# Kernel optimization log

Measured on AMD Instinct MI355X. Metric: run time of the kernel, lower is better.

Reference implementation:

```python
import jax, jax.numpy as jnp
import numpy as np

N_NODES = 50000
N_EDGES = 800000
EMBED_ROWS = 100000
NUM_RELS = 16
NUM_BASES = 4
FEAT_DIM = 32
OUT_DIM = 32
ATTN_DIM = 32


def setup_inputs() -> dict:
    key = jax.random.key(0)
    ks = jax.random.split(key, 16)
    inp = {
        'feat': jax.random.normal(ks[0], (N_NODES, FEAT_DIM), jnp.float32),
        'embed_table': jax.random.normal(ks[1], (EMBED_ROWS, FEAT_DIM), jnp.float32),
        'transform': jax.random.normal(ks[2], (FEAT_DIM * 2, OUT_DIM), jnp.float32) * 0.1,
        'weight': jax.random.normal(ks[3], (NUM_BASES, OUT_DIM, OUT_DIM), jnp.float32) * 0.1,
        'w_comp': jax.random.normal(ks[4], (NUM_RELS, NUM_BASES), jnp.float32) * 0.5,
        'self_loop_weight': jax.random.normal(ks[5], (OUT_DIM, OUT_DIM), jnp.float32) * 0.1,
        'A_w': jax.random.normal(ks[6], (2 * OUT_DIM + ATTN_DIM, OUT_DIM), jnp.float32) * 0.1,
        'A_b': jax.random.normal(ks[7], (OUT_DIM,), jnp.float32) * 0.1,
        'B_w': jax.random.normal(ks[8], (OUT_DIM, 1), jnp.float32) * 0.1,
        'B_b': jax.random.normal(ks[9], (1,), jnp.float32) * 0.1,
        'attn_emb': jax.random.normal(ks[10], (NUM_RELS, ATTN_DIM), jnp.float32),
        'idx': jax.random.randint(ks[11], (N_NODES,), 0, EMBED_ROWS, jnp.int32),
        'edge_src': jax.random.randint(ks[12], (N_EDGES,), 0, N_NODES, jnp.int32),
        'edge_dst': jax.random.randint(ks[13], (N_EDGES,), 0, N_NODES, jnp.int32),
        'edge_type': jax.random.randint(ks[14], (N_EDGES,), 0, NUM_RELS, jnp.int32),
    }
    return inp


def reference(feat, embed_table, transform, weight, w_comp, self_loop_weight,
              A_w, A_b, B_w, B_b, attn_emb, idx, edge_src, edge_dst, edge_type):
    n = feat.shape[0]
    # input-layer features: concat(feat, embed[idx]) @ transform -> init_fea [N, D]
    init_fea = jnp.concatenate([feat, embed_table[idx]], axis=1) @ transform
    # basis decomposition: rel_w [R, D, D]
    rel_w = jnp.einsum('rb,bio->rio', w_comp, weight)
    # per-edge gather (is_input_layer & add_transe_emb -> x=src init_fea, y=dst init_fea)
    x = init_fea[edge_src]                      # [E, D]
    y = init_fea[edge_dst]                      # [E, D]
    w_e = rel_w[edge_type]                      # [E, D, D]
    msg = jnp.einsum('ed,edo->eo', x, w_e)      # per-edge bmm (edge weight w = 1)
    # attention MLP: a = sigmoid(B(relu(A([x, y, rel_emb]))))
    e = jnp.concatenate([x, y, attn_emb[edge_type]], axis=1)  # [E, 2D+A]
    a = jax.nn.sigmoid(jax.nn.relu(e @ A_w + A_b) @ B_w + B_b)  # [E, 1]
    # scatter-reduce: h_v = curr_emb_v + sum_{e: dst=v} a_e * msg_e
    agg = jax.ops.segment_sum(a * msg, edge_dst, num_segments=n)
    curr = init_fea @ self_loop_weight
    h = jax.nn.relu(curr + agg)  # activation=relu, bias=None, dropout=0
    # is_input_layer & add_transe_emb: repr = concat(init_fea, h) -> [N, 2, D]
    return jnp.stack([init_fea, h], axis=1)
```

## Files before the change

### kernel.cpp

```cpp
#include <hip/hip_runtime.h>
#include <math.h>

#define NN 50000
#define NE 800000
#define NR 16
#define NEP_MAX (NE + NR * 16)
#define NB 196
#define NBIN 212
#define ABLK 256
#define CHUNK ((NE + ABLK - 1) / ABLK)

typedef __attribute__((ext_vector_type(8))) short short8;
typedef __attribute__((ext_vector_type(4))) float floatx4;

__device__ __forceinline__ unsigned short f2bf(float x) {
    unsigned int u = __float_as_uint(x);
    u += 0x7fffu + ((u >> 16) & 1u);
    return (unsigned short)(u >> 16);
}
__device__ __forceinline__ float bf2f(unsigned short s) {
    return __uint_as_float(((unsigned int)s) << 16);
}

__global__ void k_pre(const float* __restrict__ feat, const float* __restrict__ emb,
                      const float* __restrict__ T, const int* __restrict__ idx,
                      const float* __restrict__ weight, const float* __restrict__ w_comp,
                      const float* __restrict__ A_w, const float* __restrict__ A_b,
                      const float* __restrict__ attn_emb,
                      float* __restrict__ out, unsigned short* __restrict__ init_bf,
                      unsigned short* __restrict__ wfrag, unsigned short* __restrict__ afrag,
                      float* __restrict__ aproj) {
    if (blockIdx.x < 64) {
        int g = blockIdx.x * 256 + threadIdx.x;
        {
            int t = g >> 10, rest = g & 1023;
            int nt = rest >> 9, l = (rest >> 3) & 63, j = rest & 7;
            int k = (l >> 4) * 8 + j, n = (l & 15) + 16 * nt;
            float acc = 0.f;
#pragma unroll
            for (int b = 0; b < 4; b++) acc += w_comp[t * 4 + b] * weight[b * 1024 + k * 32 + n];
            wfrag[g] = f2bf(acc);
        }
        if (g < 2 * 2 * 64 * 8) {
            int ks = g >> 10, rest = g & 1023;
            int nt = rest >> 9, l = (rest >> 3) & 63, j = rest & 7;
            int k = ks * 32 + (l >> 4) * 8 + j, n = (l & 15) + 16 * nt;
            afrag[g] = f2bf(A_w[k * 32 + n]);
        }
        if (g < 16 * 32) {
            int t = g >> 5, j = g & 31;
            float acc = A_b[j];
#pragma unroll
            for (int k = 0; k < 32; k++) acc += attn_emb[t * 32 + k] * A_w[(64 + k) * 32 + j];
            aproj[g] = acc;
        }
        return;
    }
    int i = (blockIdx.x - 64) * 256 + threadIdx.x;
    if (i >= NN) return;
    float v[32], acc[32];
#pragma unroll
    for (int o = 0; o < 32; o++) acc[o] = 0.f;
    const float4* fp = (const float4*)(feat + (size_t)i * 32);
#pragma unroll
    for (int q = 0; q < 8; q++) {
        float4 f = fp[q];
        v[4 * q] = f.x; v[4 * q + 1] = f.y; v[4 * q + 2] = f.z; v[4 * q + 3] = f.w;
    }
#pragma unroll
    for (int d = 0; d < 32; d++) {
        float xd = v[d];
#pragma unroll
        for (int o = 0; o < 32; o++) acc[o] += xd * T[d * 32 + o];
    }
    int row = idx[i];
    const float4* ep = (const float4*)(emb + (size_t)row * 32);
#pragma unroll
    for (int q = 0; q < 8; q++) {
        float4 f = ep[q];
        v[4 * q] = f.x; v[4 * q + 1] = f.y; v[4 * q + 2] = f.z; v[4 * q + 3] = f.w;
    }
#pragma unroll
    for (int d = 0; d < 32; d++) {
        float xd = v[d];
#pragma unroll
        for (int o = 0; o < 32; o++) acc[o] += xd * T[(32 + d) * 32 + o];
    }
    float4* op = (float4*)(out + (size_t)i * 64);
#pragma unroll
    for (int q = 0; q < 8; q++) {
        float4 f;
        f.x = acc[4 * q]; f.y = acc[4 * q + 1]; f.z = acc[4 * q + 2]; f.w = acc[4 * q + 3];
        op[q] = f;
    }
    unsigned int w[16];
#pragma unroll
    for (int q = 0; q < 16; q++)
        w[q] = (unsigned int)f2bf(acc[2 * q]) | ((unsigned int)f2bf(acc[2 * q + 1]) << 16);
    uint4* bp = (uint4*)(init_bf + (size_t)i * 32);
#pragma unroll
    for (int q = 0; q < 4; q++) {
        uint4 u; u.x = w[4 * q]; u.y = w[4 * q + 1]; u.z = w[4 * q + 2]; u.w = w[4 * q + 3];
        bp[q] = u;
    }
}

__global__ void __launch_bounds__(1024) k_count(const int* __restrict__ ed,
                                                const int* __restrict__ et,
                                                int* __restrict__ cpb) {
    __shared__ int lc[NBIN];
    for (int i = threadIdx.x; i < NBIN; i += 1024) lc[i] = 0;
    __syncthreads();
    const int start = blockIdx.x * CHUNK, end = min(start + CHUNK, NE);
    for (int e = start + threadIdx.x; e < end; e += 1024) {
        atomicAdd(&lc[ed[e] >> 8], 1);
        atomicAdd(&lc[NB + et[e]], 1);
    }
    __syncthreads();
    for (int i = threadIdx.x; i < NBIN; i += 1024) cpb[blockIdx.x * NBIN + i] = lc[i];
}

__global__ void __launch_bounds__(256) k_scanB(const int* __restrict__ cpb,
                                               int* __restrict__ cpbx,
                                               int* __restrict__ boff,
                                               int* __restrict__ toff,
                                               int* __restrict__ tend) {
    __shared__ int tot[NBIN];
    int bin = threadIdx.x;
    if (bin < NBIN) {
        int run = 0;
#pragma unroll 8
        for (int c = 0; c < ABLK; c++) {
            int v = cpb[c * NBIN + bin];
            cpbx[c * NBIN + bin] = run;
            run += v;
        }
        tot[bin] = run;
    }
    __syncthreads();
    if (threadIdx.x == 0) {
        int acc = 0;
        for (int b = 0; b < NB; b++) { boff[b] = acc; acc += tot[b]; }
        boff[NB] = acc;
        int t0 = 0;
        for (int t = 0; t < NR; t++) {
            toff[t] = t0;
            tend[t] = t0 + tot[NB + t];
            t0 += ((tot[NB + t] + 15) >> 4) << 4;
        }
        toff[NR] = t0;
    }
}

__global__ void __launch_bounds__(1024) k_scatA(const int* __restrict__ es,
                                                const int* __restrict__ ed,
                                                const int* __restrict__ et,
                                                const int* __restrict__ cpbx,
                                                const int* __restrict__ boff,
                                                const int* __restrict__ toff,
                                                int* __restrict__ tsrc,
                                                int* __restrict__ tdst,
                                                int* __restrict__ bpack) {
    __shared__ int cur[NBIN];
    const int start = blockIdx.x * CHUNK, end = min(start + CHUNK, NE);
    for (int i = threadIdx.x; i < NBIN; i += 1024) {
        int base = (i < NB) ? boff[i] : toff[i - NB];
        cur[i] = base + cpbx[blockIdx.x * NBIN + i];
    }
    __syncthreads();
    for (int e = start + threadIdx.x; e < end; e += 1024) {
        int s = es[e], d = ed[e], t = et[e];
        int q = atomicAdd(&cur[NB + t], 1);
        int slot = atomicAdd(&cur[d >> 8], 1);
        tsrc[q] = s;
        tdst[q] = d;
        bpack[slot] = (q << 8) | (d & 255);
    }
}

__global__ void __launch_bounds__(256) k_fine(const int* __restrict__ boff,
                                              const int* __restrict__ bpack,
                                              int* __restrict__ row_off,
                                              int* __restrict__ p_of_q) {
    __shared__ int h[256], ls[256];
    const int b = blockIdx.x;
    const int s0 = boff[b], s1 = boff[b + 1];
    const int tid = threadIdx.x;
    h[tid] = 0;
    __syncthreads();
    for (int s = s0 + tid; s < s1; s += 256)
        atomicAdd(&h[bpack[s] & 255], 1);
    __syncthreads();
    int v = h[tid];
    ls[tid] = v;
    __syncthreads();
    for (int off = 1; off < 256; off <<= 1) {
        int t = (tid >= off) ? ls[tid - off] : 0;
        __syncthreads();
        ls[tid] += t;
        __syncthreads();
    }
    int excl = ls[tid] - v;
    int node = b * 256 + tid;
    if (node <= NN) row_off[node] = s0 + excl;
    h[tid] = s0 + excl;
    __syncthreads();
    for (int s = s0 + tid; s < s1; s += 256) {
        int pk = bpack[s];
        int p = atomicAdd(&h[pk & 255], 1);
        p_of_q[pk >> 8] = p;
    }
}

__global__ void __launch_bounds__(256) k_msg(
    const unsigned short* __restrict__ wfrag, const unsigned short* __restrict__ afrag,
    const float* __restrict__ aproj, const float* __restrict__ B_w,
    const float* __restrict__ B_b, const int* __restrict__ toff,
    const int* __restrict__ tend, const int* __restrict__ tsrc,
    const int* __restrict__ tdst, const int* __restrict__ p_of_q,
    const unsigned short* __restrict__ init_bf, unsigned short* __restrict__ amsg) {
    const int wave = threadIdx.x >> 6;
    const int lane = threadIdx.x & 63;
    const int q0 = (blockIdx.x * 4 + wave) * 16;
    if (q0 >= toff[NR]) return;
    int t = 0;
#pragma unroll
    for (int i = 1; i < NR; i++) t += (q0 >= toff[i]) ? 1 : 0;
    t = __builtin_amdgcn_readfirstlane(t);
    const int te = tend[t];
    const int m = lane & 15, quad = lane >> 4;
    const int qa = q0 + m;
    const bool va = qa < te;
    int src = va ? tsrc[qa] : 0;
    int dst = va ? tdst[qa] : 0;
    short8 xa = *(const short8*)(init_bf + (size_t)src * 32 + quad * 8);
    short8 ya = *(const short8*)(init_bf + (size_t)dst * 32 + quad * 8);
    short8 wb0 = *(const short8*)(wfrag + (size_t)((t * 2 + 0) * 64 + lane) * 8);
    short8 wb1 = *(const short8*)(wfrag + (size_t)((t * 2 + 1) * 64 + lane) * 8);
    short8 a00 = *(const short8*)(afrag + (size_t)((0 * 2 + 0) * 64 + lane) * 8);
    short8 a01 = *(const short8*)(afrag + (size_t)((0 * 2 + 1) * 64 + lane) * 8);
    short8 a10 = *(const short8*)(afrag + (size_t)((1 * 2 + 0) * 64 + lane) * 8);
    short8 a11 = *(const short8*)(afrag + (size_t)((1 * 2 + 1) * 64 + lane) * 8);
    floatx4 z4 = {0.f, 0.f, 0.f, 0.f};
    floatx4 mc0 = __builtin_amdgcn_mfma_f32_16x16x32_bf16(xa, wb0, z4, 0, 0, 0);
    floatx4 mc1 = __builtin_amdgcn_mfma_f32_16x16x32_bf16(xa, wb1, z4, 0, 0, 0);
    floatx4 hc0 = __builtin_amdgcn_mfma_f32_16x16x32_bf16(xa, a00, z4, 0, 0, 0);
    hc0 = __builtin_amdgcn_mfma_f32_16x16x32_bf16(ya, a10, hc0, 0, 0, 0);
    floatx4 hc1 = __builtin_amdgcn_mfma_f32_16x16x32_bf16(xa, a01, z4, 0, 0, 0);
    hc1 = __builtin_amdgcn_mfma_f32_16x16x32_bf16(ya, a11, hc1, 0, 0, 0);
    const int col = m;
    float ap0 = aproj[t * 32 + col], ap1 = aproj[t * 32 + 16 + col];
    float bw0 = B_w[col], bw1 = B_w[col + 16];
    float bb = B_b[0];
    float part[4];
#pragma unroll
    for (int r = 0; r < 4; r++)
        part[r] = fmaxf(hc0[r] + ap0, 0.f) * bw0 + fmaxf(hc1[r] + ap1, 0.f) * bw1;
#pragma unroll
    for (int s = 1; s < 16; s <<= 1) {
#pragma unroll
        for (int r = 0; r < 4; r++) part[r] += __shfl_xor(part[r], s, 64);
    }
#pragma unroll
    for (int r = 0; r < 4; r++) {
        int qe = q0 + quad * 4 + r;
        if (qe < te) {
            int pe = p_of_q[qe];
            float a = 1.f / (1.f + __expf(-(part[r] + bb)));
            amsg[(size_t)pe * 32 + col] = f2bf(a * mc0[r]);
            amsg[(size_t)pe * 32 + col + 16] = f2bf(a * mc1[r]);
        }
    }
}

__global__ void __launch_bounds__(256) k_agg(
    const int* __restrict__ row_off, const unsigned short* __restrict__ amsg,
    const float* __restrict__ S, float* __restrict__ out) {
    int tid = threadIdx.x;
    int v = blockIdx.x * 64 + (tid >> 2);
    if (v >= NN) return;
    int c0 = (tid & 3) * 8;
    float acc[8];
#pragma unroll
    for (int j = 0; j < 8; j++) acc[j] = 0.f;
    int p0 = row_off[v], p1 = row_off[v + 1];
    for (int p = p0; p < p1; p++) {
        short8 mv = *(const short8*)(amsg + (size_t)p * 32 + c0);
#pragma unroll
        for (int j = 0; j < 8; j++) acc[j] += bf2f((unsigned short)mv[j]);
    }
    float x[32];
    const float4* xp = (const float4*)(out + (size_t)v * 64);
#pragma unroll
    for (int q = 0; q < 8; q++) {
        float4 f = xp[q];
        x[4 * q] = f.x; x[4 * q + 1] = f.y; x[4 * q + 2] = f.z; x[4 * q + 3] = f.w;
    }
#pragma unroll
    for (int d = 0; d < 32; d++) {
        float xd = x[d];
#pragma unroll
        for (int j = 0; j < 8; j++) acc[j] += xd * S[d * 32 + c0 + j];
    }
    float4* op = (float4*)(out + (size_t)v * 64 + 32 + c0);
#pragma unroll
    for (int q = 0; q < 2; q++) {
        float4 f;
        f.x = fmaxf(acc[4 * q], 0.f);
        f.y = fmaxf(acc[4 * q + 1], 0.f);
        f.z = fmaxf(acc[4 * q + 2], 0.f);
        f.w = fmaxf(acc[4 * q + 3], 0.f);
        op[q] = f;
    }
}

extern "C" void kernel_launch(void* const* d_in, const int* in_sizes, int n_in,
                              void* d_out, int out_size, void* d_ws, size_t ws_size,
                              hipStream_t stream) {
    const float* feat      = (const float*)d_in[0];
    const float* embed     = (const float*)d_in[1];
    const float* transform = (const float*)d_in[2];
    const float* weight    = (const float*)d_in[3];
    const float* w_comp    = (const float*)d_in[4];
    const float* self_w    = (const float*)d_in[5];
    const float* A_w       = (const float*)d_in[6];
    const float* A_b       = (const float*)d_in[7];
    const float* B_w       = (const float*)d_in[8];
    const float* B_b       = (const float*)d_in[9];
    const float* attn_emb  = (const float*)d_in[10];
    const int*   idx       = (const int*)d_in[11];
    const int*   edge_src  = (const int*)d_in[12];
    const int*   edge_dst  = (const int*)d_in[13];
    const int*   edge_type = (const int*)d_in[14];
    float* out = (float*)d_out;

    char* ws = (char*)d_ws;
    unsigned short* amsg    = (unsigned short*)ws;
    int*            bpack   = (int*)ws;
    unsigned short* init_bf = (unsigned short*)(ws + (size_t)NEP_MAX * 64);
    unsigned short* wfrag   = (unsigned short*)((char*)init_bf + 3200000);
    unsigned short* afrag   = (unsigned short*)((char*)wfrag + 32768);
    float*          aproj   = (float*)((char*)afrag + 4096);
    int* ip       = (int*)((char*)aproj + 2048);
    int* toff     = ip;              ip += 32;
    int* tend     = ip;              ip += 16;
    int* boff     = ip;              ip += 200;
    int* cpb      = ip;              ip += ABLK * NBIN;
    int* cpbx     = ip;              ip += ABLK * NBIN;
    int* row_off  = ip;              ip += NN + 1;
    int* tsrc     = ip;              ip += NEP_MAX;
    int* tdst     = ip;              ip += NEP_MAX;
    int* p_of_q   = ip;              ip += NEP_MAX;

    k_pre<<<260, 256, 0, stream>>>(feat, embed, transform, idx, weight, w_comp,
                                   A_w, A_b, attn_emb, out, init_bf, wfrag, afrag, aproj);
    k_count<<<ABLK, 1024, 0, stream>>>(edge_dst, edge_type, cpb);
    k_scanB<<<1, 256, 0, stream>>>(cpb, cpbx, boff, toff, tend);
    k_scatA<<<ABLK, 1024, 0, stream>>>(edge_src, edge_dst, edge_type, cpbx, boff, toff,
                                       tsrc, tdst, bpack);
    k_fine<<<NB, 256, 0, stream>>>(boff, bpack, row_off, p_of_q);
    const int tiles = NEP_MAX / 16;
    k_msg<<<(tiles + 3) / 4, 256, 0, stream>>>(wfrag, afrag, aproj, B_w, B_b,
                                               toff, tend, tsrc, tdst, p_of_q,
                                               init_bf, amsg);
    k_agg<<<(NN + 63) / 64, 256, 0, stream>>>(row_off, amsg, self_w, out);
}
```

Baseline: 214.4 us.

## Fuse message and aggregation per 64-node bucket with shared-memory atomics

Replaces the type-sorted edge layout, the fine per-node sort, the bf16 message buffer and the separate aggregation kernel with one kernel per 64-destination bucket. It computes the messages for all four bases with MFMA, combines them with per-edge w_comp, and accumulates into shared memory with atomics. It also folds the dst-bin counting into the preprocessing launch and packs src, local dst and type into one int. This removes several kernels and large intermediate global traffic, at the cost of four times the basis MFMAs and shared-memory atomic contention. The packed form assumes src fits in 16 bits, but node ids go up to 50000, which is below 65536, so it holds.

```diff
diff --git a/kernel.cpp b/kernel.cpp
--- a/kernel.cpp
+++ b/kernel.cpp
@@ -4,9 +4,8 @@
 #define NN 50000
 #define NE 800000
 #define NR 16
-#define NEP_MAX (NE + NR * 16)
-#define NB 196
-#define NBIN 212
+#define BNODE 64
+#define NBC 782
 #define ABLK 256
 #define CHUNK ((NE + ABLK - 1) / ABLK)
 
@@ -18,28 +17,35 @@
     u += 0x7fffu + ((u >> 16) & 1u);
     return (unsigned short)(u >> 16);
 }
-__device__ __forceinline__ float bf2f(unsigned short s) {
-    return __uint_as_float(((unsigned int)s) << 16);
-}
-
-__global__ void k_pre(const float* __restrict__ feat, const float* __restrict__ emb,
-                      const float* __restrict__ T, const int* __restrict__ idx,
-                      const float* __restrict__ weight, const float* __restrict__ w_comp,
-                      const float* __restrict__ A_w, const float* __restrict__ A_b,
-                      const float* __restrict__ attn_emb,
-                      float* __restrict__ out, unsigned short* __restrict__ init_bf,
-                      unsigned short* __restrict__ wfrag, unsigned short* __restrict__ afrag,
-                      float* __restrict__ aproj) {
+
+__global__ void __launch_bounds__(256) k_pre(
+    const float* __restrict__ feat, const float* __restrict__ emb,
+    const float* __restrict__ T, const int* __restrict__ idx,
+    const float* __restrict__ weight, const float* __restrict__ A_w,
+    const float* __restrict__ A_b, const float* __restrict__ attn_emb,
+    const int* __restrict__ ed,
+    float* __restrict__ out, unsigned short* __restrict__ init_bf,
+    unsigned short* __restrict__ bfrag, unsigned short* __restrict__ afrag,
+    float* __restrict__ aproj, int* __restrict__ cpb) {
+    if (blockIdx.x >= 260) {
+        __shared__ int lc[NBC];
+        const int cb = blockIdx.x - 260;
+        for (int i = threadIdx.x; i < NBC; i += 256) lc[i] = 0;
+        __syncthreads();
+        const int start = cb * CHUNK, end = min(start + CHUNK, NE);
+        for (int e = start + threadIdx.x; e < end; e += 256)
+            atomicAdd(&lc[ed[e] >> 6], 1);
+        __syncthreads();
+        for (int i = threadIdx.x; i < NBC; i += 256) cpb[cb * NBC + i] = lc[i];
+        return;
+    }
     if (blockIdx.x < 64) {
         int g = blockIdx.x * 256 + threadIdx.x;
-        {
-            int t = g >> 10, rest = g & 1023;
-            int nt = rest >> 9, l = (rest >> 3) & 63, j = rest & 7;
-            int k = (l >> 4) * 8 + j, n = (l & 15) + 16 * nt;
-            float acc = 0.f;
-#pragma unroll
-            for (int b = 0; b < 4; b++) acc += w_comp[t * 4 + b] * weight[b * 1024 + k * 32 + n];
-            wfrag[g] = f2bf(acc);
+        if (g < 4 * 2 * 64 * 8) {
+            int b2 = g >> 10, rest = g & 1023;
+            int h = rest >> 9, l = (rest >> 3) & 63, j = rest & 7;
+            int k = (l >> 4) * 8 + j, n = (l & 15) + 16 * h;
+            bfrag[g] = f2bf(weight[b2 * 1024 + k * 32 + n]);
         }
         if (g < 2 * 2 * 64 * 8) {
             int ks = g >> 10, rest = g & 1023;
@@ -105,34 +111,16 @@
     }
 }
 
-__global__ void __launch_bounds__(1024) k_count(const int* __restrict__ ed,
-                                                const int* __restrict__ et,
-                                                int* __restrict__ cpb) {
-    __shared__ int lc[NBIN];
-    for (int i = threadIdx.x; i < NBIN; i += 1024) lc[i] = 0;
-    __syncthreads();
-    const int start = blockIdx.x * CHUNK, end = min(start + CHUNK, NE);
-    for (int e = start + threadIdx.x; e < end; e += 1024) {
-        atomicAdd(&lc[ed[e] >> 8], 1);
-        atomicAdd(&lc[NB + et[e]], 1);
-    }
-    __syncthreads();
-    for (int i = threadIdx.x; i < NBIN; i += 1024) cpb[blockIdx.x * NBIN + i] = lc[i];
-}
-
 __global__ void __launch_bounds__(256) k_scanB(const int* __restrict__ cpb,
                                                int* __restrict__ cpbx,
-                                               int* __restrict__ boff,
-                                               int* __restrict__ toff,
-                                               int* __restrict__ tend) {
-    __shared__ int tot[NBIN];
-    int bin = threadIdx.x;
-    if (bin < NBIN) {
+                                               int* __restrict__ boff) {
+    __shared__ int tot[NBC];
+    for (int bin = threadIdx.x; bin < NBC; bin += 256) {
         int run = 0;
 #pragma unroll 8
         for (int c = 0; c < ABLK; c++) {
-            int v = cpb[c * NBIN + bin];
-            cpbx[c * NBIN + bin] = run;
+            int v = cpb[c * NBC + bin];
+            cpbx[c * NBC + bin] = run;
             run += v;
         }
         tot[bin] = run;
@@ -140,15 +128,9 @@
     __syncthreads();
     if (threadIdx.x == 0) {
         int acc = 0;
-        for (int b = 0; b < NB; b++) { boff[b] = acc; acc += tot[b]; }
-        boff[NB] = acc;
-        int t0 = 0;
-        for (int t = 0; t < NR; t++) {
-            toff[t] = t0;
-            tend[t] = t0 + tot[NB + t];
-            t0 += ((tot[NB + t] + 15) >> 4) << 4;
-        }
-        toff[NR] = t0;
+#pragma unroll 8
+        for (int b = 0; b < NBC; b++) { boff[b] = acc; acc += tot[b]; }
+        boff[NBC] = acc;
     }
 }
 
@@ -157,138 +139,102 @@
                                                 const int* __restrict__ et,
                                                 const int* __restrict__ cpbx,
                                                 const int* __restrict__ boff,
-                                                const int* __restrict__ toff,
-                                                int* __restrict__ tsrc,
-                                                int* __restrict__ tdst,
                                                 int* __restrict__ bpack) {
-    __shared__ int cur[NBIN];
+    __shared__ int cur[NBC];
     const int start = blockIdx.x * CHUNK, end = min(start + CHUNK, NE);
-    for (int i = threadIdx.x; i < NBIN; i += 1024) {
-        int base = (i < NB) ? boff[i] : toff[i - NB];
-        cur[i] = base + cpbx[blockIdx.x * NBIN + i];
-    }
+    for (int i = threadIdx.x; i < NBC; i += 1024)
+        cur[i] = boff[i] + cpbx[blockIdx.x * NBC + i];
     __syncthreads();
-    for (int e = start + threadIdx.x; e < end; e += 1024) {
+    for (int e = start + threadIdx.x; e += 0, e < end; e += 1024) {
         int s = es[e], d = ed[e], t = et[e];
-        int q = atomicAdd(&cur[NB + t], 1);
-        int slot = atomicAdd(&cur[d >> 8], 1);
-        tsrc[q] = s;
-        tdst[q] = d;
-        bpack[slot] = (q << 8) | (d & 255);
-    }
-}
-
-__global__ void __launch_bounds__(256) k_fine(const int* __restrict__ boff,
-                                              const int* __restrict__ bpack,
-                                              int* __restrict__ row_off,
-                                              int* __restrict__ p_of_q) {
-    __shared__ int h[256], ls[256];
+        int slot = atomicAdd(&cur[d >> 6], 1);
+        bpack[slot] = s | ((d & 63) << 16) | (t << 22);
+    }
+}
+
+__global__ void __launch_bounds__(256) k_msgagg(
+    const unsigned short* __restrict__ bfrag, const unsigned short* __restrict__ afrag,
+    const float* __restrict__ aproj, const float* __restrict__ w_comp,
+    const float* __restrict__ B_w, const float* __restrict__ B_b,
+    const int* __restrict__ boff, const int* __restrict__ bpack,
+    const unsigned short* __restrict__ init_bf, const float* __restrict__ S,
+    float* __restrict__ out) {
+    __shared__ float acc[BNODE * 33];
+    const int tid = threadIdx.x, lane = tid & 63, wave = tid >> 6;
     const int b = blockIdx.x;
+    for (int i = tid; i < BNODE * 33; i += 256) acc[i] = 0.f;
     const int s0 = boff[b], s1 = boff[b + 1];
-    const int tid = threadIdx.x;
-    h[tid] = 0;
+    const int m = lane & 15, quad = lane >> 4;
+    const short8* bfp = (const short8*)bfrag;
+    short8 wb00 = bfp[(0 * 2 + 0) * 64 + lane];
+    short8 wb01 = bfp[(0 * 2 + 1) * 64 + lane];
+    short8 wb10 = bfp[(1 * 2 + 0) * 64 + lane];
+    short8 wb11 = bfp[(1 * 2 + 1) * 64 + lane];
+    short8 wb20 = bfp[(2 * 2 + 0) * 64 + lane];
+    short8 wb21 = bfp[(2 * 2 + 1) * 64 + lane];
+    short8 wb30 = bfp[(3 * 2 + 0) * 64 + lane];
+    short8 wb31 = bfp[(3 * 2 + 1) * 64 + lane];
+    const short8* afp = (const short8*)afrag;
+    short8 a00 = afp[(0 * 2 + 0) * 64 + lane];
+    short8 a01 = afp[(0 * 2 + 1) * 64 + lane];
+    short8 a10 = afp[(1 * 2 + 0) * 64 + lane];
+    short8 a11 = afp[(1 * 2 + 1) * 64 + lane];
+    const float bw0 = B_w[m], bw1 = B_w[m + 16], bb = B_b[0];
     __syncthreads();
-    for (int s = s0 + tid; s < s1; s += 256)
-        atomicAdd(&h[bpack[s] & 255], 1);
+    const int ntile = (s1 - s0 + 15) >> 4;
+    for (int ti = wave; ti < ntile; ti += 4) {
+        const int e0 = s0 + ti * 16;
+        const int ea = e0 + m;
+        int pk = (ea < s1) ? bpack[ea] : 0;
+        int src = pk & 0xffff;
+        int dst = (b << 6) + ((pk >> 16) & 63);
+        short8 xa = *(const short8*)(init_bf + (size_t)src * 32 + quad * 8);
+        short8 ya = *(const short8*)(init_bf + (size_t)dst * 32 + quad * 8);
+        floatx4 z4 = {0.f, 0.f, 0.f, 0.f};
+        floatx4 hc0 = __builtin_amdgcn_mfma_f32_16x16x32_bf16(xa, a00, z4, 0, 0, 0);
+        hc0 = __builtin_amdgcn_mfma_f32_16x16x32_bf16(ya, a10, hc0, 0, 0, 0);
+        floatx4 hc1 = __builtin_amdgcn_mfma_f32_16x16x32_bf16(xa, a01, z4, 0, 0, 0);
+        hc1 = __builtin_amdgcn_mfma_f32_16x16x32_bf16(ya, a11, hc1, 0, 0, 0);
+        floatx4 zb00 = __builtin_amdgcn_mfma_f32_16x16x32_bf16(xa, wb00, z4, 0, 0, 0);
+        floatx4 zb10 = __builtin_amdgcn_mfma_f32_16x16x32_bf16(xa, wb10, z4, 0, 0, 0);
+        floatx4 zb20 = __builtin_amdgcn_mfma_f32_16x16x32_bf16(xa, wb20, z4, 0, 0, 0);
+        floatx4 zb30 = __builtin_amdgcn_mfma_f32_16x16x32_bf16(xa, wb30, z4, 0, 0, 0);
+        floatx4 zb01 = __builtin_amdgcn_mfma_f32_16x16x32_bf16(xa, wb01, z4, 0, 0, 0);
+        floatx4 zb11 = __builtin_amdgcn_mfma_f32_16x16x32_bf16(xa, wb11, z4, 0, 0, 0);
+        floatx4 zb21 = __builtin_amdgcn_mfma_f32_16x16x32_bf16(xa, wb21, z4, 0, 0, 0);
+        floatx4 zb31 = __builtin_amdgcn_mfma_f32_16x16x32_bf16(xa, wb31, z4, 0, 0, 0);
+        int pkr[4];
+        float part[4];
+#pragma unroll
+        for (int r = 0; r < 4; r++) {
+            pkr[r] = __shfl(pk, quad * 20 + r, 64);
+            int t_r = (pkr[r] >> 22) & 15;
+            part[r] = fmaxf(hc0[r] + aproj[t_r * 32 + m], 0.f) * bw0
+                    + fmaxf(hc1[r] + aproj[t_r * 32 + 16 + m], 0.f) * bw1;
+        }
+#pragma unroll
+        for (int s = 1; s < 16; s <<= 1) {
+#pragma unroll
+            for (int r = 0; r < 4; r++) part[r] += __shfl_xor(part[r], s, 64);
+        }
+#pragma unroll
+        for (int r = 0; r < 4; r++) {
+            if (e0 + quad * 4 + r < s1) {
+                int t_r = (pkr[r] >> 22) & 15;
+                int f_r = (pkr[r] >> 16) & 63;
+                const float4 wc = *(const float4*)(w_comp + t_r * 4);
+                float a = 1.f / (1.f + __expf(-(part[r] + bb)));
+                float m0 = wc.x * zb00[r] + wc.y * zb10[r] + wc.z * zb20[r] + wc.w * zb30[r];
+                float m1 = wc.x * zb01[r] + wc.y * zb11[r] + wc.z * zb21[r] + wc.w * zb31[r];
+                atomicAdd(&acc[f_r * 33 + m], a * m0);
+                atomicAdd(&acc[f_r * 33 + 16 + m], a * m1);
+            }
+        }
+    }
     __syncthreads();
-    int v = h[tid];
-    ls[tid] = v;
-    __syncthreads();
-    for (int off = 1; off < 256; off <<= 1) {
-        int t = (tid >= off) ? ls[tid - off] : 0;
-        __syncthreads();
-        ls[tid] += t;
-        __syncthreads();
-    }
-    int excl = ls[tid] - v;
-    int node = b * 256 + tid;
-    if (node <= NN) row_off[node] = s0 + excl;
-    h[tid] = s0 + excl;
-    __syncthreads();
-    for (int s = s0 + tid; s < s1; s += 256) {
-        int pk = bpack[s];
-        int p = atomicAdd(&h[pk & 255], 1);
-        p_of_q[pk >> 8] = p;
-    }
-}
-
-__global__ void __launch_bounds__(256) k_msg(
-    const unsigned short* __restrict__ wfrag, const unsigned short* __restrict__ afrag,
-    const float* __restrict__ aproj, const float* __restrict__ B_w,
-    const float* __restrict__ B_b, const int* __restrict__ toff,
-    const int* __restrict__ tend, const int* __restrict__ tsrc,
-    const int* __restrict__ tdst, const int* __restrict__ p_of_q,
-    const unsigned short* __restrict__ init_bf, unsigned short* __restrict__ amsg) {
-    const int wave = threadIdx.x >> 6;
-    const int lane = threadIdx.x & 63;
-    const int q0 = (blockIdx.x * 4 + wave) * 16;
-    if (q0 >= toff[NR]) return;
-    int t = 0;
-#pragma unroll
-    for (int i = 1; i < NR; i++) t += (q0 >= toff[i]) ? 1 : 0;
-    t = __builtin_amdgcn_readfirstlane(t);
-    const int te = tend[t];
-    const int m = lane & 15, quad = lane >> 4;
-    const int qa = q0 + m;
-    const bool va = qa < te;
-    int src = va ? tsrc[qa] : 0;
-    int dst = va ? tdst[qa] : 0;
-    short8 xa = *(const short8*)(init_bf + (size_t)src * 32 + quad * 8);
-    short8 ya = *(const short8*)(init_bf + (size_t)dst * 32 + quad * 8);
-    short8 wb0 = *(const short8*)(wfrag + (size_t)((t * 2 + 0) * 64 + lane) * 8);
-    short8 wb1 = *(const short8*)(wfrag + (size_t)((t * 2 + 1) * 64 + lane) * 8);
-    short8 a00 = *(const short8*)(afrag + (size_t)((0 * 2 + 0) * 64 + lane) * 8);
-    short8 a01 = *(const short8*)(afrag + (size_t)((0 * 2 + 1) * 64 + lane) * 8);
-    short8 a10 = *(const short8*)(afrag + (size_t)((1 * 2 + 0) * 64 + lane) * 8);
-    short8 a11 = *(const short8*)(afrag + (size_t)((1 * 2 + 1) * 64 + lane) * 8);
-    floatx4 z4 = {0.f, 0.f, 0.f, 0.f};
-    floatx4 mc0 = __builtin_amdgcn_mfma_f32_16x16x32_bf16(xa, wb0, z4, 0, 0, 0);
-    floatx4 mc1 = __builtin_amdgcn_mfma_f32_16x16x32_bf16(xa, wb1, z4, 0, 0, 0);
-    floatx4 hc0 = __builtin_amdgcn_mfma_f32_16x16x32_bf16(xa, a00, z4, 0, 0, 0);
-    hc0 = __builtin_amdgcn_mfma_f32_16x16x32_bf16(ya, a10, hc0, 0, 0, 0);
-    floatx4 hc1 = __builtin_amdgcn_mfma_f32_16x16x32_bf16(xa, a01, z4, 0, 0, 0);
-    hc1 = __builtin_amdgcn_mfma_f32_16x16x32_bf16(ya, a11, hc1, 0, 0, 0);
-    const int col = m;
-    float ap0 = aproj[t * 32 + col], ap1 = aproj[t * 32 + 16 + col];
-    float bw0 = B_w[col], bw1 = B_w[col + 16];
-    float bb = B_b[0];
-    float part[4];
-#pragma unroll
-    for (int r = 0; r < 4; r++)
-        part[r] = fmaxf(hc0[r] + ap0, 0.f) * bw0 + fmaxf(hc1[r] + ap1, 0.f) * bw1;
-#pragma unroll
-    for (int s = 1; s < 16; s <<= 1) {
-#pragma unroll
-        for (int r = 0; r < 4; r++) part[r] += __shfl_xor(part[r], s, 64);
-    }
-#pragma unroll
-    for (int r = 0; r < 4; r++) {
-        int qe = q0 + quad * 4 + r;
-        if (qe < te) {
-            int pe = p_of_q[qe];
-            float a = 1.f / (1.f + __expf(-(part[r] + bb)));
-            amsg[(size_t)pe * 32 + col] = f2bf(a * mc0[r]);
-            amsg[(size_t)pe * 32 + col + 16] = f2bf(a * mc1[r]);
-        }
-    }
-}
-
-__global__ void __launch_bounds__(256) k_agg(
-    const int* __restrict__ row_off, const unsigned short* __restrict__ amsg,
-    const float* __restrict__ S, float* __restrict__ out) {
-    int tid = threadIdx.x;
-    int v = blockIdx.x * 64 + (tid >> 2);
+    const int vl = tid >> 2, c0 = (tid & 3) * 8;
+    const int v = b * BNODE + vl;
     if (v >= NN) return;
-    int c0 = (tid & 3) * 8;
-    float acc[8];
-#pragma unroll
-    for (int j = 0; j < 8; j++) acc[j] = 0.f;
-    int p0 = row_off[v], p1 = row_off[v + 1];
-    for (int p = p0; p < p1; p++) {
-        short8 mv = *(const short8*)(amsg + (size_t)p * 32 + c0);
-#pragma unroll
-        for (int j = 0; j < 8; j++) acc[j] += bf2f((unsigned short)mv[j]);
-    }
     float x[32];
     const float4* xp = (const float4*)(out + (size_t)v * 64);
 #pragma unroll
@@ -296,20 +242,23 @@
         float4 f = xp[q];
         x[4 * q] = f.x; x[4 * q + 1] = f.y; x[4 * q + 2] = f.z; x[4 * q + 3] = f.w;
     }
+    float av[8];
+#pragma unroll
+    for (int j = 0; j < 8; j++) av[j] = acc[vl * 33 + c0 + j];
 #pragma unroll
     for (int d = 0; d < 32; d++) {
         float xd = x[d];
 #pragma unroll
-        for (int j = 0; j < 8; j++) acc[j] += xd * S[d * 32 + c0 + j];
+        for (int j = 0; j < 8; j++) av[j] += xd * S[d * 32 + c0 + j];
     }
     float4* op = (float4*)(out + (size_t)v * 64 + 32 + c0);
 #pragma unroll
     for (int q = 0; q < 2; q++) {
         float4 f;
-        f.x = fmaxf(acc[4 * q], 0.f);
-        f.y = fmaxf(acc[4 * q + 1], 0.f);
-        f.z = fmaxf(acc[4 * q + 2], 0.f);
-        f.w = fmaxf(acc[4 * q + 3], 0.f);
+        f.x = fmaxf(av[4 * q], 0.f);
+        f.y = fmaxf(av[4 * q + 1], 0.f);
+        f.z = fmaxf(av[4 * q + 2], 0.f);
+        f.w = fmaxf(av[4 * q + 3], 0.f);
         op[q] = f;
     }
 }
@@ -335,33 +284,21 @@
     float* out = (float*)d_out;
 
     char* ws = (char*)d_ws;
-    unsigned short* amsg    = (unsigned short*)ws;
-    int*            bpack   = (int*)ws;
-    unsigned short* init_bf = (unsigned short*)(ws + (size_t)NEP_MAX * 64);
-    unsigned short* wfrag   = (unsigned short*)((char*)init_bf + 3200000);
-    unsigned short* afrag   = (unsigned short*)((char*)wfrag + 32768);
-    float*          aproj   = (float*)((char*)afrag + 4096);
-    int* ip       = (int*)((char*)aproj + 2048);
-    int* toff     = ip;              ip += 32;
-    int* tend     = ip;              ip += 16;
-    int* boff     = ip;              ip += 200;
-    int* cpb      = ip;              ip += ABLK * NBIN;
-    int* cpbx     = ip;              ip += ABLK * NBIN;
-    int* row_off  = ip;              ip += NN + 1;
-    int* tsrc     = ip;              ip += NEP_MAX;
-    int* tdst     = ip;              ip += NEP_MAX;
-    int* p_of_q   = ip;              ip += NEP_MAX;
-
-    k_pre<<<260, 256, 0, stream>>>(feat, embed, transform, idx, weight, w_comp,
-                                   A_w, A_b, attn_emb, out, init_bf, wfrag, afrag, aproj);
-    k_count<<<ABLK, 1024, 0, stream>>>(edge_dst, edge_type, cpb);
-    k_scanB<<<1, 256, 0, stream>>>(cpb, cpbx, boff, toff, tend);
-    k_scatA<<<ABLK, 1024, 0, stream>>>(edge_src, edge_dst, edge_type, cpbx, boff, toff,
-                                       tsrc, tdst, bpack);
-    k_fine<<<NB, 256, 0, stream>>>(boff, bpack, row_off, p_of_q);
-    const int tiles = NEP_MAX / 16;
-    k_msg<<<(tiles + 3) / 4, 256, 0, stream>>>(wfrag, afrag, aproj, B_w, B_b,
-                                               toff, tend, tsrc, tdst, p_of_q,
-                                               init_bf, amsg);
-    k_agg<<<(NN + 63) / 64, 256, 0, stream>>>(row_off, amsg, self_w, out);
-}
+    unsigned short* init_bf = (unsigned short*)ws;
+    unsigned short* bfrag   = (unsigned short*)(ws + 3200000);
+    unsigned short* afrag   = (unsigned short*)(ws + 3208192);
+    float*          aproj   = (float*)(ws + 3212288);
+    int* ip      = (int*)(ws + 3214336);
+    int* boff    = ip;            ip += NBC + 2;
+    int* cpb     = ip;            ip += ABLK * NBC;
+    int* cpbx    = ip;            ip += ABLK * NBC;
+    int* bpack   = ip;            ip += NE;
+
+    k_pre<<<516, 256, 0, stream>>>(feat, embed, transform, idx, weight,
+                                   A_w, A_b, attn_emb, edge_dst,
+                                   out, init_bf, bfrag, afrag, aproj, cpb);
+    k_scanB<<<1, 256, 0, stream>>>(cpb, cpbx, boff);
+    k_scatA<<<ABLK, 1024, 0, stream>>>(edge_src, edge_dst, edge_type, cpbx, boff, bpack);
+    k_msgagg<<<NBC, 256, 0, stream>>>(bfrag, afrag, aproj, w_comp, B_w, B_b,
+                                      boff, bpack, init_bf, self_w, out);
+}
```

Measured after the change: 381.0 us. 77.7% more time.
